# Optimization experiments

Measured on AMD Instinct MI355X. Metric: run time of the kernel, lower is better.

The kernel has to match this reference:

```python
import jax, jax.numpy as jnp
import numpy as np

TAPS = 5
DELAY = 3
EPS_POWER = 1e-7   # clamp for inverse power (wpe_one_iteration eps)
EPS_REG = 1e-10    # diagonal loading of the correlation matrix


def setup_inputs() -> dict:
    key = jax.random.key(0)
    ks = jax.random.split(key, 5)
    B, F, C, T = 8, 257, 8, 800
    shp = (B, F, C, T)
    return {
        "data_sep_real": jax.random.normal(ks[0], shp, jnp.float32),
        "data_sep_imag": jax.random.normal(ks[1], shp, jnp.float32),
        "data_mix_real": jax.random.normal(ks[2], shp, jnp.float32),
        "data_mix_imag": jax.random.normal(ks[3], shp, jnp.float32),
        "ilens": jax.random.randint(ks[4], (B,), 1, T + 1, jnp.int32),
    }


def _ytilde(Y, taps, delay):
    # Y: (B,F,C,T) complex -> stacked delayed taps (B,F,taps*C,T)
    # tap k at time t holds Y[..., t - delay - k] (zero-padded past)
    B, F, C, T = Y.shape
    Yp = jnp.pad(Y, ((0, 0), (0, 0), (0, 0), (delay + taps - 1, 0)))
    tilde = jnp.stack(
        [Yp[..., taps - 1 - k: taps - 1 - k + T] for k in range(taps)], axis=2
    )  # (B,F,taps,C,T)
    return tilde.reshape(B, F, taps * C, T)


def _wpe_one_iteration(Y, power, taps, delay):
    # Y: (B,F,C,T) complex, power: (B,F,T) real
    B, F, C, T = Y.shape
    inv_power = 1.0 / jnp.maximum(power, EPS_POWER)          # (B,F,T)
    Yt = _ytilde(Y, taps, delay)                              # (B,F,K,T), K=taps*C
    t0 = delay + taps - 1                                     # correlations use t >= t0
    Ytv = Yt[..., t0:]
    Yv = Y[..., t0:]
    Ytw = Ytv * inv_power[:, :, None, t0:].astype(Y.dtype)
    # R = sum_t w(t) Ytilde(t) Ytilde(t)^H  -> (B,F,K,K)
    R = jnp.einsum('bfat,bfct->bfac', Ytw, jnp.conj(Ytv))
    # P = sum_t w(t) Ytilde(t) Y(t)^H      -> (B,F,K,C)
    P = jnp.einsum('bfat,bfet->bfae', Ytw, jnp.conj(Yv))
    K = taps * C
    R = R + EPS_REG * jnp.eye(K, dtype=R.dtype)
    G = jnp.linalg.solve(R, P)                                # (B,F,K,C)
    # X(t) = Y(t) - G^H Ytilde(t)
    X = Y - jnp.einsum('bfae,bfat->bfet', jnp.conj(G), Yt)
    return X


def reference(data_sep_real, data_sep_imag, data_mix_real, data_mix_imag, ilens):
    # power of separated signal, averaged over channels (use_dnn_mask=False)
    power = jnp.mean(data_sep_real ** 2 + data_sep_imag ** 2, axis=-2)  # (B,F,T)
    Ym = jax.lax.complex(data_mix_real, data_mix_imag)                  # (B,F,C,T)
    X = _wpe_one_iteration(Ym, power, TAPS, DELAY)
    # zero out padded frames: t >= ilens[b]
    t = jnp.arange(X.shape[-1])
    valid = t[None, :] < ilens[:, None]                                 # (B,T)
    X = jnp.where(valid[:, None, None, :], X, 0)
    # return real/imag stacked on last axis: (B,F,C,T,2)
    return jnp.stack([X.real, X.imag], axis=-1)
```

## Files before the change

kernel.cpp:

```cpp
#include <hip/hip_runtime.h>

#define B 8
#define F 257
#define C 8
#define T 800
#define TAPS 5
#define DELAY 3
#define K 40
#define NCOL 48
#define T0 7
#define BF (B*F)

typedef __bf16 bf16x8 __attribute__((ext_vector_type(8)));
typedef __bf16 bf16x4 __attribute__((ext_vector_type(4)));
typedef float f32x4 __attribute__((ext_vector_type(4)));

struct PF { float4 v[3]; };

__device__ __forceinline__ void dma16(const void* g, void* l) {
    __builtin_amdgcn_global_load_lds(
        (const __attribute__((address_space(1))) void*)g,
        (__attribute__((address_space(3))) void*)l, 16, 0, 0);
}

__global__ __launch_bounds__(256) void power_kernel(const float* __restrict__ sr,
                                                    const float* __restrict__ si,
                                                    float* __restrict__ W) {
    int bf = blockIdx.x;
    const float* srp = sr + (size_t)bf * C * T;
    const float* sip = si + (size_t)bf * C * T;
    int t0 = threadIdx.x * 4;
    if (t0 < T) {
        float s[4] = {0.f, 0.f, 0.f, 0.f};
#pragma unroll
        for (int c = 0; c < C; ++c) {
            float4 a = *(const float4*)(srp + c * T + t0);
            float4 b = *(const float4*)(sip + c * T + t0);
            s[0] = fmaf(a.x, a.x, fmaf(b.x, b.x, s[0]));
            s[1] = fmaf(a.y, a.y, fmaf(b.y, b.y, s[1]));
            s[2] = fmaf(a.z, a.z, fmaf(b.z, b.z, s[2]));
            s[3] = fmaf(a.w, a.w, fmaf(b.w, b.w, s[3]));
        }
        float4 w;
        float* wp = (float*)&w;
#pragma unroll
        for (int e = 0; e < 4; ++e) {
            float v = fmaxf(s[e] * (1.0f / C), 1e-7f);
            wp[e] = (t0 + e < T0) ? 0.f : rsqrtf(v);
        }
        *(float4*)(W + (size_t)bf * T + t0) = w;
    }
}

#define WB2 13824

__global__ __launch_bounds__(256, 2) void rp_mfma_kernel(const float* __restrict__ mr,
                                                         const float* __restrict__ mi,
                                                         const float* __restrict__ W,
                                                         float2* __restrict__ Rout,
                                                         float2* __restrict__ Pout) {
    __shared__ __align__(16) unsigned char SH[4 * WB2];
    const int lane = threadIdx.x & 63;
    const int wid = threadIdx.x >> 6;
    const int bf = blockIdx.x * 4 + wid;
    unsigned char* base = SH + wid * WB2;
    unsigned char* b0 = base + 7680;
    unsigned char* b1 = base + 10752;

    const float* mrp = mr + (size_t)bf * C * T;
    const float* mip = mi + (size_t)bf * C * T;
    const float* Wp  = W  + (size_t)bf * T;

    const int q = lane >> 4, col = lane & 15;
    const int pc = lane >> 3, pg = lane & 7;

    const int PM[6] = {0, 0, 0, 1, 1, 2};
    const int PN[6] = {0, 1, 2, 1, 2, 2};

    const float* sb[3];
    const float* sb0[3];
    bool hal[3];
#pragma unroll
    for (int it = 0; it < 3; ++it) {
        int task = lane + it * 64;
        hal[it] = false;
        if (task < 160) {
            int row = task / 10, grp = task - row * 10;
            int pl = row >> 3, c = row & 7;
            const float* cb = (pl ? mip : mrp) + c * T;
            sb[it] = cb + grp * 4 - 8;
            hal[it] = (grp < 2);
            sb0[it] = hal[it] ? cb : sb[it];
        } else if (task < 168) {
            sb[it] = Wp + (task - 160) * 4;
            sb0[it] = sb[it];
        } else {
            sb[it] = mrp + (task - 168) * 4;
            sb0[it] = sb[it];
        }
    }

    f32x4 accRe[6], accIr[6], accRi[6];
#pragma unroll
    for (int p = 0; p < 6; ++p) {
        accRe[p] = (f32x4){0.f, 0.f, 0.f, 0.f};
        accIr[p] = (f32x4){0.f, 0.f, 0.f, 0.f};
        accRi[p] = (f32x4){0.f, 0.f, 0.f, 0.f};
    }

#pragma unroll
    for (int it = 0; it < 3; ++it)
        dma16(sb0[it], b0 + (lane + it * 64) * 16);
    asm volatile("s_waitcnt vmcnt(0)" ::: "memory");
#pragma unroll
    for (int it = 0; it < 3; ++it) {
        int task = lane + it * 64;
        if (hal[it])
            *(float4*)(b0 + task * 16) = make_float4(0.f, 0.f, 0.f, 0.f);
    }
    __builtin_amdgcn_sched_barrier(0);

    for (int ks = 0; ks < 25; ++ks) {
        unsigned char* buf = (ks & 1) ? b1 : b0;
        unsigned char* nbuf = (ks & 1) ? b0 : b1;
        int ntb = (ks < 24) ? (ks + 1) * 32 : ks * 32;
#pragma unroll
        for (int it = 0; it < 3; ++it)
            dma16(sb[it] + ntb, nbuf + (lane + it * 64) * 16);
        asm volatile("s_waitcnt vmcnt(3)" ::: "memory");
        __builtin_amdgcn_sched_barrier(0);

        {
            const float* yrr = (const float*)(buf + pc * 160);
            const float* yir = (const float*)(buf + (8 + pc) * 160);
            float yre[12], yim[12];
            float4 r0 = *(const float4*)(yrr + pg * 4);
            float4 r1 = *(const float4*)(yrr + pg * 4 + 4);
            float4 r2 = *(const float4*)(yrr + pg * 4 + 8);
            float4 i0 = *(const float4*)(yir + pg * 4);
            float4 i1 = *(const float4*)(yir + pg * 4 + 4);
            float4 i2 = *(const float4*)(yir + pg * 4 + 8);
            yre[0] = r0.x; yre[1] = r0.y; yre[2]  = r0.z; yre[3]  = r0.w;
            yre[4] = r1.x; yre[5] = r1.y; yre[6]  = r1.z; yre[7]  = r1.w;
            yre[8] = r2.x; yre[9] = r2.y; yre[10] = r2.z; yre[11] = r2.w;
            yim[0] = i0.x; yim[1] = i0.y; yim[2]  = i0.z; yim[3]  = i0.w;
            yim[4] = i1.x; yim[5] = i1.y; yim[6]  = i1.z; yim[7]  = i1.w;
            yim[8] = i2.x; yim[9] = i2.y; yim[10] = i2.z; yim[11] = i2.w;
            float4 w4 = *(const float4*)(buf + 2560 + pg * 16);
            float wv[4] = {w4.x, w4.y, w4.z, w4.w};
#pragma unroll
            for (int v = 0; v < 6; ++v) {
                int row = (v < 5) ? (v * 8 + pc) : (40 + pc);
                int off = (v < 5) ? (5 - v) : 8;
                bf16x4 zr, zi;
#pragma unroll
                for (int e = 0; e < 4; ++e) {
                    zr[e] = (__bf16)(wv[e] * yre[off + e]);
                    zi[e] = (__bf16)(wv[e] * yim[off + e]);
                }
                *(bf16x4*)(base + row * 80 + pg * 8) = zr;
                *(bf16x4*)(base + 3840 + row * 80 + pg * 8) = zi;
            }
        }

        bf16x8 fr[3], fi[3];
#pragma unroll
        for (int X = 0; X < 3; ++X) {
            fr[X] = *(const bf16x8*)(base + (X * 16 + col) * 80 + q * 16);
            fi[X] = *(const bf16x8*)(base + 3840 + (X * 16 + col) * 80 + q * 16);
        }
#pragma unroll
        for (int p = 0; p < 6; ++p) {
            int mt = PM[p], nt = PN[p];
            accRe[p] = __builtin_amdgcn_mfma_f32_16x16x32_bf16(fr[mt], fr[nt], accRe[p], 0, 0, 0);
            accRe[p] = __builtin_amdgcn_mfma_f32_16x16x32_bf16(fi[mt], fi[nt], accRe[p], 0, 0, 0);
            accIr[p] = __builtin_amdgcn_mfma_f32_16x16x32_bf16(fi[mt], fr[nt], accIr[p], 0, 0, 0);
            accRi[p] = __builtin_amdgcn_mfma_f32_16x16x32_bf16(fr[mt], fi[nt], accRi[p], 0, 0, 0);
        }
    }

    float2* Rp = Rout + (size_t)bf * K * K;
    float2* Pp = Pout + (size_t)bf * K * C;
#pragma unroll
    for (int p = 0; p < 6; ++p) {
        int mt = PM[p], nt = PN[p];
#pragma unroll
        for (int r = 0; r < 4; ++r) {
            int m = mt * 16 + q * 4 + r;
            int n = nt * 16 + col;
            float re = accRe[p][r];
            float im = accIr[p][r] - accRi[p][r];
            if (m < K) {
                if (n < K) {
                    if (m == n) re += 1e-10f;
                    Rp[m * K + n] = make_float2(re, im);
                } else {
                    Pp[m * C + (n - K)] = make_float2(re, im);
                }
            }
            if (mt != nt && m < K && n < K)
                Rp[n * K + m] = make_float2(re, -im);
        }
    }
}

__device__ __forceinline__ float rdlane(float v, int j) {
    return __uint_as_float(__builtin_amdgcn_readlane(__float_as_uint(v), (unsigned)j));
}

__global__ __launch_bounds__(64, 2) void solve_kernel(const float2* __restrict__ Rin,
                                                      const float2* __restrict__ Pin,
                                                      float2* __restrict__ Gout) {
    const int bf = blockIdx.x;
    const int lane = threadIdx.x;
    const bool act = lane < K;

    float2 row[NCOL];
    {
        const float4* Rp4 = (const float4*)(Rin + (size_t)bf * K * K + (size_t)(act ? lane : 0) * K);
        const float4* Pp4 = (const float4*)(Pin + (size_t)bf * K * C + (size_t)(act ? lane : 0) * C);
#pragma unroll
        for (int m = 0; m < K / 2; ++m) {
            float4 v = Rp4[m];
            if (!act) v = make_float4(0.f, 0.f, 0.f, 0.f);
            row[2 * m]     = make_float2(v.x, v.y);
            row[2 * m + 1] = make_float2(v.z, v.w);
        }
#pragma unroll
        for (int m = 0; m < C / 2; ++m) {
            float4 v = Pp4[m];
            if (!act) v = make_float4(0.f, 0.f, 0.f, 0.f);
            row[K + 2 * m]     = make_float2(v.x, v.y);
            row[K + 2 * m + 1] = make_float2(v.z, v.w);
        }
    }

#pragma unroll
    for (int j = 0; j < K; ++j) {
        float dx = rdlane(row[j].x, j);
        float dy = rdlane(row[j].y, j);
        float den = fmaf(dx, dx, dy * dy);
        float r = 1.0f / den;
        float ix = dx * r;
        float iy = -dy * r;
        float lx = row[j].x * ix - row[j].y * iy;
        float ly = row[j].x * iy + row[j].y * ix;
        bool isj = (lane == j);
        lx = isj ? (1.0f - ix) : lx;
        ly = isj ? (0.0f - iy) : ly;
#pragma unroll
        for (int n = j; n < NCOL; ++n) {
            float ux = rdlane(row[n].x, j);
            float uy = rdlane(row[n].y, j);
            row[n].x = fmaf(-lx, ux, fmaf( ly, uy, row[n].x));
            row[n].y = fmaf(-lx, uy, fmaf(-ly, ux, row[n].y));
        }
    }

    if (act) {
        float4* Gp = (float4*)(Gout + (size_t)bf * K * C + (size_t)lane * C);
#pragma unroll
        for (int m = 0; m < C / 2; ++m)
            Gp[m] = make_float4(row[K + 2 * m].x, row[K + 2 * m].y,
                                row[K + 2 * m + 1].x, row[K + 2 * m + 1].y);
    }
}

#define XSTR 144
#define XWB 12032

__device__ __forceinline__ PF x_load(const float* __restrict__ mrp,
                                     const float* __restrict__ mip,
                                     int tb, int lane) {
    PF p;
#pragma unroll
    for (int it = 0; it < 3; ++it) {
        int task = lane + it * 64;
        float4 v = make_float4(0.f, 0.f, 0.f, 0.f);
        if (task < 160) {
            int pl = task / 80;
            int rem = task - pl * 80;
            int c = rem / 10, grp = rem - c * 10;
            int tg = tb - 8 + grp * 4;
            const float* srcp = pl ? mip : mrp;
            if (tg >= 0) v = *(const float4*)(srcp + c * T + tg);
        }
        p.v[it] = v;
    }
    return p;
}

__device__ __forceinline__ void x_store(const PF& p, float* sre, float* sim_, int lane) {
#pragma unroll
    for (int it = 0; it < 3; ++it) {
        int task = lane + it * 64;
        if (task < 160) {
            int pl = task / 80;
            int rem = task - pl * 80;
            int c = rem / 10, grp = rem - c * 10;
            *(float4*)((pl ? sim_ : sre) + c * 44 + grp * 4) = p.v[it];
        }
    }
}

__global__ __launch_bounds__(64) void x_mfma_kernel(const float* __restrict__ mr,
                                                    const float* __restrict__ mi,
                                                    const float2* __restrict__ Gin,
                                                    const int* __restrict__ ilens,
                                                    float2* __restrict__ out) {
    __shared__ __align__(16) unsigned char SH[XWB];
    const int lane = threadIdx.x;
    const int gid = blockIdx.x;
    const int bf = gid >> 2;
    const int split = gid & 3;
    const int ck0 = (split == 0) ? 0 : (1 + split * 6);
    const int nck = (split == 0) ? 7 : 6;
    unsigned char* base = SH;
    float* sre = (float*)(base + 9216);
    float* sim_ = (float*)(base + 10624);

    const float* mrp = mr + (size_t)bf * C * T;
    const float* mip = mi + (size_t)bf * C * T;
    const float2* Gp = Gin + (size_t)bf * K * C;
    float2* outp = out + (size_t)bf * C * T;
    const int len = ilens[bf / F];

    const int q = lane >> 4, col = lane & 15;
    const int t2 = lane >> 1, half = lane & 1;

#pragma unroll
    for (int pl = 0; pl < 2; ++pl) {
        unsigned char* pb = base + pl * 4608 + t2 * XSTR + 80 + half * 24;
        *(float2*)(pb)      = make_float2(0.f, 0.f);
        *(float2*)(pb + 8)  = make_float2(0.f, 0.f);
        *(float2*)(pb + 16) = make_float2(0.f, 0.f);
    }

    bf16x8 Agr[2], Agi[2], Agin[2];
#pragma unroll
    for (int ks = 0; ks < 2; ++ks)
#pragma unroll
        for (int j = 0; j < 8; ++j) {
            int a = ks * 32 + q * 8 + j;
            float2 g = make_float2(0.f, 0.f);
            if (a < K && col < C) g = Gp[a * C + col];
            Agr[ks][j]  = (__bf16)g.x;
            Agi[ks][j]  = (__bf16)g.y;
            Agin[ks][j] = (__bf16)(-g.y);
        }

    PF cur = x_load(mrp, mip, ck0 * 32, lane);

    for (int ci = 0; ci < nck; ++ci) {
        const int tb = (ck0 + ci) * 32;

        x_store(cur, sre, sim_, lane);
        if (ci + 1 < nck) cur = x_load(mrp, mip, tb + 32, lane);

#pragma unroll
        for (int i = 0; i < 5; ++i) {
            int abase = half * 20 + 4 * i;
            bf16x4 zr, zi;
#pragma unroll
            for (int e2 = 0; e2 < 4; ++e2) {
                int a = abase + e2;
                int v = a >> 3, c = a & 7;
                int idx = c * 44 + t2 + 5 - v;
                zr[e2] = (__bf16)sre[idx];
                zi[e2] = (__bf16)sim_[idx];
            }
            *(bf16x4*)(base + t2 * XSTR + abase * 2) = zr;
            *(bf16x4*)(base + 4608 + t2 * XSTR + abase * 2) = zi;
        }

#pragma unroll
        for (int tt = 0; tt < 2; ++tt) {
            const int trow = tt * 16 + col;
            f32x4 accRe = (f32x4){0.f, 0.f, 0.f, 0.f};
            f32x4 accIm = (f32x4){0.f, 0.f, 0.f, 0.f};
#pragma unroll
            for (int ks = 0; ks < 2; ++ks) {
                bf16x8 byr = *(const bf16x8*)(base + trow * XSTR + ks * 64 + q * 16);
                bf16x8 byi = *(const bf16x8*)(base + 4608 + trow * XSTR + ks * 64 + q * 16);
                accRe = __builtin_amdgcn_mfma_f32_16x16x32_bf16(Agr[ks], byr, accRe, 0, 0, 0);
                accRe = __builtin_amdgcn_mfma_f32_16x16x32_bf16(Agi[ks], byi, accRe, 0, 0, 0);
                accIm = __builtin_amdgcn_mfma_f32_16x16x32_bf16(Agr[ks], byi, accIm, 0, 0, 0);
                accIm = __builtin_amdgcn_mfma_f32_16x16x32_bf16(Agin[ks], byr, accIm, 0, 0, 0);
            }
            if (q < 2) {
                int t = tb + tt * 16 + col;
                int l = tt * 16 + col + 8;
                bool ok = (t < len);
#pragma unroll
                for (int r = 0; r < 4; ++r) {
                    int e = q * 4 + r;
                    float yr = sre[e * 44 + l];
                    float yi = sim_[e * 44 + l];
                    float2 v = ok ? make_float2(yr - accRe[r], yi - accIm[r])
                                  : make_float2(0.f, 0.f);
                    outp[e * T + t] = v;
                }
            }
        }
    }
}

extern "C" void kernel_launch(void* const* d_in, const int* in_sizes, int n_in,
                              void* d_out, int out_size, void* d_ws, size_t ws_size,
                              hipStream_t stream) {
    const float* sep_r = (const float*)d_in[0];
    const float* sep_i = (const float*)d_in[1];
    const float* mix_r = (const float*)d_in[2];
    const float* mix_i = (const float*)d_in[3];
    const int* ilens   = (const int*)d_in[4];

    float* ws = (float*)d_ws;
    float* W = ws;
    float2* Rws = (float2*)(ws + (size_t)BF * T);
    float2* Gws = Rws + (size_t)BF * K * K;

    power_kernel<<<BF, 256, 0, stream>>>(sep_r, sep_i, W);
    rp_mfma_kernel<<<BF / 4, 256, 0, stream>>>(mix_r, mix_i, W, Rws, Gws);
    solve_kernel<<<BF, 64, 0, stream>>>(Rws, Gws, Gws);
    x_mfma_kernel<<<BF * 4, 64, 0, stream>>>(mix_r, mix_i, Gws, ilens, (float2*)d_out);
}
```

Baseline: 181.3 us.

## Split Gauss-Jordan solve columns across four wavefronts with LDS-broadcast multipliers

```diff
diff --git a/kernel.cpp b/kernel.cpp
--- a/kernel.cpp
+++ b/kernel.cpp
@@ -208,61 +208,69 @@
     return __uint_as_float(__builtin_amdgcn_readlane(__float_as_uint(v), (unsigned)j));
 }
 
-__global__ __launch_bounds__(64, 2) void solve_kernel(const float2* __restrict__ Rin,
-                                                      const float2* __restrict__ Pin,
-                                                      float2* __restrict__ Gout) {
+__global__ __launch_bounds__(256) void solve_kernel(const float2* __restrict__ Rin,
+                                                    const float2* __restrict__ Pin,
+                                                    float2* __restrict__ Gout) {
+    __shared__ float2 lbuf[2][64];
     const int bf = blockIdx.x;
-    const int lane = threadIdx.x;
+    const int lane = threadIdx.x & 63;
+    const int w = threadIdx.x >> 6;
     const bool act = lane < K;
-
-    float2 row[NCOL];
+    const int lr = act ? lane : 0;
+
+    float2 colw[12];
     {
-        const float4* Rp4 = (const float4*)(Rin + (size_t)bf * K * K + (size_t)(act ? lane : 0) * K);
-        const float4* Pp4 = (const float4*)(Pin + (size_t)bf * K * C + (size_t)(act ? lane : 0) * C);
-#pragma unroll
-        for (int m = 0; m < K / 2; ++m) {
-            float4 v = Rp4[m];
-            if (!act) v = make_float4(0.f, 0.f, 0.f, 0.f);
-            row[2 * m]     = make_float2(v.x, v.y);
-            row[2 * m + 1] = make_float2(v.z, v.w);
-        }
-#pragma unroll
-        for (int m = 0; m < C / 2; ++m) {
-            float4 v = Pp4[m];
-            if (!act) v = make_float4(0.f, 0.f, 0.f, 0.f);
-            row[K + 2 * m]     = make_float2(v.x, v.y);
-            row[K + 2 * m + 1] = make_float2(v.z, v.w);
+        const float2* Arow = Rin + (size_t)bf * K * K + (size_t)lr * K;
+        const float2* Prow = Pin + (size_t)bf * K * C + (size_t)lr * C;
+#pragma unroll
+        for (int m = 0; m < 10; ++m) {
+            float2 v = Arow[4 * m + w];
+            colw[m] = act ? v : make_float2(0.f, 0.f);
+        }
+#pragma unroll
+        for (int m = 10; m < 12; ++m) {
+            float2 v = Prow[4 * (m - 10) + w];
+            colw[m] = act ? v : make_float2(0.f, 0.f);
         }
     }
 
 #pragma unroll
     for (int j = 0; j < K; ++j) {
-        float dx = rdlane(row[j].x, j);
-        float dy = rdlane(row[j].y, j);
-        float den = fmaf(dx, dx, dy * dy);
-        float r = 1.0f / den;
-        float ix = dx * r;
-        float iy = -dy * r;
-        float lx = row[j].x * ix - row[j].y * iy;
-        float ly = row[j].x * iy + row[j].y * ix;
-        bool isj = (lane == j);
-        lx = isj ? (1.0f - ix) : lx;
-        ly = isj ? (0.0f - iy) : ly;
-#pragma unroll
-        for (int n = j; n < NCOL; ++n) {
-            float ux = rdlane(row[n].x, j);
-            float uy = rdlane(row[n].y, j);
-            row[n].x = fmaf(-lx, ux, fmaf( ly, uy, row[n].x));
-            row[n].y = fmaf(-lx, uy, fmaf(-ly, ux, row[n].y));
+        const int par = j & 1;
+        const int wo = j & 3;
+        const int mj = j >> 2;
+        if (w == wo) {
+            float dx = rdlane(colw[mj].x, j);
+            float dy = rdlane(colw[mj].y, j);
+            float den = fmaf(dx, dx, dy * dy);
+            float r = 1.0f / den;
+            float ix = dx * r, iy = -dy * r;
+            float lx = colw[mj].x * ix - colw[mj].y * iy;
+            float ly = colw[mj].x * iy + colw[mj].y * ix;
+            bool isj = (lane == j);
+            lx = isj ? (1.0f - ix) : lx;
+            ly = isj ? (0.0f - iy) : ly;
+            lbuf[par][lane] = make_float2(lx, ly);
+        }
+        __syncthreads();
+        float2 l = lbuf[par][lane];
+#pragma unroll
+        for (int m = 0; m < 12; ++m) {
+            if (4 * m + 3 <= j) continue;
+            bool doit = (4 * m > j) || (4 * m + w > j);
+            if (doit) {
+                float ux = rdlane(colw[m].x, j);
+                float uy = rdlane(colw[m].y, j);
+                colw[m].x = fmaf(-l.x, ux, fmaf( l.y, uy, colw[m].x));
+                colw[m].y = fmaf(-l.x, uy, fmaf(-l.y, ux, colw[m].y));
+            }
         }
     }
 
     if (act) {
-        float4* Gp = (float4*)(Gout + (size_t)bf * K * C + (size_t)lane * C);
-#pragma unroll
-        for (int m = 0; m < C / 2; ++m)
-            Gp[m] = make_float4(row[K + 2 * m].x, row[K + 2 * m].y,
-                                row[K + 2 * m + 1].x, row[K + 2 * m + 1].y);
+        float2* Gp = Gout + (size_t)bf * K * C + (size_t)lane * C;
+        Gp[w]     = colw[10];
+        Gp[4 + w] = colw[11];
     }
 }
 
@@ -421,6 +429,6 @@
 
     power_kernel<<<BF, 256, 0, stream>>>(sep_r, sep_i, W);
     rp_mfma_kernel<<<BF / 4, 256, 0, stream>>>(mix_r, mix_i, W, Rws, Gws);
-    solve_kernel<<<BF, 64, 0, stream>>>(Rws, Gws, Gws);
+    solve_kernel<<<BF, 256, 0, stream>>>(Rws, Gws, Gws);
     x_mfma_kernel<<<BF * 4, 64, 0, stream>>>(mix_r, mix_i, Gws, ilens, (float2*)d_out);
 }
```

After: 182.0 us. About the same (+0.4%).
